# Performance work log

Measured on AMD Instinct MI355X. Metric: run time of the kernel, lower is better.

Reference implementation:

```python
import jax
import jax.numpy as jnp
import numpy as np
from jax.scipy.linalg import expm

H = 2048   # hidden_size
R = 1      # low-rank dimension
B = 2048   # batch of independent (h, x) pairs


def _glorot(key, shape):
    return jax.random.uniform(key, shape, minval=-1.0, maxval=1.0) * jnp.sqrt(2.0 / sum(shape))


def setup_inputs() -> dict:
    key = jax.random.key(0)
    k1, k2, k3, k4, k5, k6 = jax.random.split(key, 6)
    return {
        "h": jax.random.normal(k5, (B, H), dtype=jnp.float32),
        "x": jax.random.normal(k6, (B, H), dtype=jnp.float32),
        # a_diag ~ U(-1, 0) * init_scale (10.0): negative real diagonal
        "a_diag": jax.random.uniform(k1, (H,), minval=-1.0, maxval=0.0) * 10.0,
        "p_vec": _glorot(k2, (H, R)),
        "q_vec": _glorot(k3, (H, R)),
        "b_mat": _glorot(k4, (H, H)),
        "delta": jnp.array(0.1, dtype=jnp.float32),
    }


def reference(h, x, a_diag, p_vec, q_vec, b_mat, delta):
    # A = diag(a_diag) + P Q^T  (DPLR structure, materialized dense as in source)
    A = jnp.diag(a_diag) + p_vec @ q_vec.T                       # [H, H]
    # Discretized state matrix: exp(delta * A)
    expA = expm(delta * A)                                       # [H, H]
    # Discretized input matrix: A^{-1} (exp(delta A) - I) B  (pinv as in source)
    A_inv = jnp.linalg.pinv(A)                                   # [H, H]
    B_disc = A_inv @ (expA - jnp.eye(H, dtype=A.dtype)) @ b_mat  # [H, H]
    # Batched recurrence step: A h + B x  for each row of h, x
    return h @ expA.T + x @ B_disc.T                             # [B, H]
```

## Files before the change

### kernel.cpp

```cpp
#include <hip/hip_runtime.h>

#define MAXM 16
#define NL_CAP 256
#define THETA 0.1f
#define SMEM_BYTES 36864

typedef unsigned short u16;
typedef u16 u16x8 __attribute__((ext_vector_type(8)));
typedef u16 u16x4 __attribute__((ext_vector_type(4)));
typedef __bf16 bf16x8 __attribute__((ext_vector_type(8)));
typedef float f32x4 __attribute__((ext_vector_type(4)));


__device__ __forceinline__ u16 f2bf(float f) {
    unsigned u = __float_as_uint(f);
    return (u16)((u + 0x7fffu + ((u >> 16) & 1u)) >> 16);
}

__global__ __launch_bounds__(256)
void conv_k(const float* __restrict__ x, const float* __restrict__ b,
            u16* __restrict__ xb, u16* __restrict__ bb, long nx, long nb)
{
    long i = ((long)blockIdx.x * 256 + threadIdx.x) * 4;
    if (i < nx) {
        float4 v = *(const float4*)&x[i];
        u16x4 o = {f2bf(v.x), f2bf(v.y), f2bf(v.z), f2bf(v.w)};
        *(u16x4*)&xb[i] = o;
    }
    if (i < nb) {
        float4 v = *(const float4*)&b[i];
        u16x4 o = {f2bf(v.x), f2bf(v.y), f2bf(v.z), f2bf(v.w)};
        *(u16x4*)&bb[i] = o;
    }
}


__device__ __forceinline__ double frcp(double den) {
    double r = (double)__builtin_amdgcn_rcpf((float)den);
    return fma(r, fma(-den, r, 1.0), r);
}


__device__ __forceinline__ void gload_lds16(const void* g, void* l) {
    __builtin_amdgcn_global_load_lds(
        (const __attribute__((address_space(1))) unsigned int*)g,
        (__attribute__((address_space(3))) unsigned int*)l, 16, 0, 0);
}

__device__ __forceinline__ void gemm_tile(u16* Al, u16* Bl, int tid, int bx, int by,
                                          const u16* __restrict__ A,
                                          const u16* __restrict__ B,
                                          float* __restrict__ C,
                                          int Ndim, int Kdim)
{
    const int bm = by * 128, bn = bx * 128;
    const int wv = tid >> 6, ln = tid & 63;
    const int wr = (wv >> 1) * 64, wc = (wv & 1) * 64;
    const int fr = ln & 15, fk = (ln >> 4) * 8;

    const int r0 = tid >> 2, c0 = (tid & 3) * 8;
    const u16* Ap0 = A + (size_t)(bm + r0) * Kdim + c0;
    const u16* Ap1 = Ap0 + (size_t)64 * Kdim;
    const u16* Bp0 = B + (size_t)(bn + r0) * Kdim + c0;
    const u16* Bp1 = Bp0 + (size_t)64 * Kdim;
    u16* AlW0 = Al + wv * 512;
    u16* AlW1 = Al + 2048 + wv * 512;
    u16* BlW0 = Bl + wv * 512;
    u16* BlW1 = Bl + 2048 + wv * 512;

    f32x4 acc[4][4];
#pragma unroll
    for (int m = 0; m < 4; ++m)
#pragma unroll
        for (int n = 0; n < 4; ++n) acc[m][n] = (f32x4)0.f;

    for (int kk = 0; kk < Kdim; kk += 32) {
        __syncthreads();
        gload_lds16(Ap0 + kk, AlW0);
        gload_lds16(Ap1 + kk, AlW1);
        gload_lds16(Bp0 + kk, BlW0);
        gload_lds16(Bp1 + kk, BlW1);
        __syncthreads();
        u16x8 af[4], bf[4];
#pragma unroll
        for (int m = 0; m < 4; ++m)
            af[m] = *(const u16x8*)&Al[(wr + m * 16 + fr) * 32 + fk];
#pragma unroll
        for (int n = 0; n < 4; ++n)
            bf[n] = *(const u16x8*)&Bl[(wc + n * 16 + fr) * 32 + fk];
#pragma unroll
        for (int m = 0; m < 4; ++m)
#pragma unroll
            for (int n = 0; n < 4; ++n)
                acc[m][n] = __builtin_amdgcn_mfma_f32_16x16x32_bf16(
                    __builtin_bit_cast(bf16x8, af[m]),
                    __builtin_bit_cast(bf16x8, bf[n]), acc[m][n], 0, 0, 0);
    }

    const int crow = (ln >> 4) * 4;
#pragma unroll
    for (int m = 0; m < 4; ++m)
#pragma unroll
        for (int n = 0; n < 4; ++n) {
            const size_t base = (size_t)(bm + wr + m * 16 + crow) * Ndim
                              + bn + wc + n * 16 + fr;
#pragma unroll
            for (int j = 0; j < 4; ++j)
                C[base + (size_t)j * Ndim] = acc[m][n][j];
        }
}

__global__ __launch_bounds__(256)
void bgemm_k(const u16* __restrict__ A, const u16* __restrict__ B,
             float* __restrict__ C, int Ndim, int Kdim)
{
    __shared__ __align__(16) unsigned char smem[SMEM_BYTES];
    gemm_tile((u16*)smem, (u16*)smem + 4096, threadIdx.x,
              blockIdx.x, blockIdx.y, A, B, C, Ndim, Kdim);
}


__global__ __launch_bounds__(256)
void g_sgemm_k(const float* __restrict__ A, const float* __restrict__ B,
               float* __restrict__ C, int Mdim, int Ndim, int Kdim)
{
    __shared__ __align__(16) float As[16][132];
    __shared__ __align__(16) float Bs[16][68];
    const int tid = threadIdx.x;
    const int tx = tid & 15, ty = tid >> 4;
    const int bn = blockIdx.x * 64, bm = blockIdx.y * 128;
    const int lrA = tid >> 1, lcA = (tid & 1) << 3;
    const int lrB = tid >> 2, lcB = (tid & 3) << 2;
    const float* Aptr = A + (size_t)(bm + lrA) * Kdim + lcA;
    const float* Bptr = B + (size_t)(bn + lrB) * Kdim + lcB;
    float4 a0 = *(const float4*)(Aptr);
    float4 a1 = *(const float4*)(Aptr + 4);
    float4 b0 = *(const float4*)(Bptr);
    float acc[8][4];
#pragma unroll
    for (int i = 0; i < 8; ++i)
#pragma unroll
        for (int j = 0; j < 4; ++j) acc[i][j] = 0.f;
    for (int kk = 0; kk < Kdim; kk += 16) {
        __syncthreads();
        As[lcA + 0][lrA] = a0.x; As[lcA + 1][lrA] = a0.y;
        As[lcA + 2][lrA] = a0.z; As[lcA + 3][lrA] = a0.w;
        As[lcA + 4][lrA] = a1.x; As[lcA + 5][lrA] = a1.y;
        As[lcA + 6][lrA] = a1.z; As[lcA + 7][lrA] = a1.w;
        Bs[lcB + 0][lrB] = b0.x; Bs[lcB + 1][lrB] = b0.y;
        Bs[lcB + 2][lrB] = b0.z; Bs[lcB + 3][lrB] = b0.w;
        __syncthreads();
        if (kk + 16 < Kdim) {
            a0 = *(const float4*)(Aptr + kk + 16);
            a1 = *(const float4*)(Aptr + kk + 20);
            b0 = *(const float4*)(Bptr + kk + 16);
        }
#pragma unroll
        for (int k = 0; k < 16; ++k) {
            const float4 av0 = *(const float4*)&As[k][ty * 8];
            const float4 av1 = *(const float4*)&As[k][ty * 8 + 4];
            const float4 bv  = *(const float4*)&Bs[k][tx * 4];
            const float avf[8] = {av0.x, av0.y, av0.z, av0.w, av1.x, av1.y, av1.z, av1.w};
            const float bvf[4] = {bv.x, bv.y, bv.z, bv.w};
#pragma unroll
            for (int i = 0; i < 8; ++i)
#pragma unroll
                for (int j = 0; j < 4; ++j) acc[i][j] += avf[i] * bvf[j];
        }
    }
#pragma unroll
    for (int i = 0; i < 8; ++i) {
        const int r = bm + ty * 8 + i;
        float4 v = {acc[i][0], acc[i][1], acc[i][2], acc[i][3]};
        *(float4*)&C[(size_t)r * Ndim + bn + tx * 4] = v;
    }
}


__device__ __forceinline__ double wsum(double x) {
#pragma unroll
    for (int m = 32; m; m >>= 1) x += __shfl_xor(x, m, 64);
    return x;
}
__device__ __forceinline__ float wsumf(float x) {
#pragma unroll
    for (int m = 32; m; m >>= 1) x += __shfl_xor(x, m, 64);
    return x;
}

__device__ __forceinline__ int inert(double s11, double s12, double s22,
                                     double dc, double cS)
{
    double b00 = cS - s11, b01 = -1.0 - s12, b11 = -s22;
    double det = b00 * b11 - b01 * b01, tr = b00 + b11;
    int neg = (det > 0.0) ? ((tr < 0.0) ? 2 : 0) : 1;
    return (int)(dc + 0.5) + neg - 1;
}

__device__ __forceinline__ int lane_evalN32(float tf, double td, int n4,
    const float4* l0, const float4* l1, const float4* l2,
    const double* pc, bool poly, double cS,
    double& g11o, double& g12o, double& g22o)
{
    float s11 = 0.f, s12 = 0.f, s22 = 0.f, dc = 0.f;
#pragma unroll 2
    for (int i = 0; i < n4; ++i) {
        const float4 d4 = l0[i], x4 = l1[i], y4 = l2[i];
        const float dd[4] = {d4.x, d4.y, d4.z, d4.w};
        const float xx[4] = {x4.x, x4.y, x4.z, x4.w};
        const float yy[4] = {y4.x, y4.y, y4.z, y4.w};
#pragma unroll
        for (int e = 0; e < 4; ++e) {
            float den = dd[e] - tf;
            float mag = fmaxf(fabsf(den), 1e-30f);
            den = (den < 0.f) ? -mag : mag;
            const float inv = __builtin_amdgcn_rcpf(den);
            s11 = fmaf(xx[e] * xx[e], inv, s11);
            s12 = fmaf(xx[e] * yy[e], inv, s12);
            s22 = fmaf(yy[e] * yy[e], inv, s22);
            if (dd[e] < tf) dc += 1.f;
        }
    }
    double S11 = (double)s11, S12 = (double)s12, S22 = (double)s22;
    if (poly) {
        S11 += pc[0] + td * (pc[3] + td * (pc[6] + td * pc[9]));
        S12 += pc[1] + td * (pc[4] + td * (pc[7] + td * pc[10]));
        S22 += pc[2] + td * (pc[5] + td * (pc[8] + td * pc[11]));
    }
    g11o = S11; g12o = S12; g22o = S22;
    return inert(S11, S12, S22, (double)dc, cS);
}

__device__ void spec256(unsigned char* smem, int tid,
                        const float* __restrict__ av, const float* __restrict__ pv,
                        const float* __restrict__ qv, double* __restrict__ hdr,
                        float* __restrict__ V)
{
    float* sd2 = (float*)smem;
    float* sw1 = sd2 + 2048;
    float* sw2 = sw1 + 2048;
    float* nl0 = sw2 + 2048;
    float* nl1 = nl0 + NL_CAP;
    float* nl2 = nl1 + NL_CAP;
    double* dsh = (double*)(nl2 + NL_CAP);
    int* ish = (int*)(dsh + 192);

    const int lane = tid & 63, wv = tid >> 6;
    const int j0 = tid * 8;

    float d2r[8], w1r[8], w2r[8];
    double cS = 0, n1 = 0, n2 = 0, mx = 0;
#pragma unroll
    for (int h = 0; h < 2; ++h) {
        float4 aa = *(const float4*)&av[j0 + h * 4];
        float4 pp = *(const float4*)&pv[j0 + h * 4];
        float4 qq = *(const float4*)&qv[j0 + h * 4];
        const float a4[4] = {aa.x, aa.y, aa.z, aa.w};
        const float p4[4] = {pp.x, pp.y, pp.z, pp.w};
        const float q4[4] = {qq.x, qq.y, qq.z, qq.w};
#pragma unroll
        for (int e = 0; e < 4; ++e) {
            const int ix = h * 4 + e;
            d2r[ix] = a4[e] * a4[e];
            w1r[ix] = a4[e] * p4[e];
            w2r[ix] = q4[e];
            sd2[j0 + ix] = d2r[ix]; sw1[j0 + ix] = w1r[ix]; sw2[j0 + ix] = w2r[ix];
            cS += (double)p4[e] * p4[e];
            n1 += (double)w1r[ix] * w1r[ix];
            n2 += (double)w2r[ix] * w2r[ix];
            mx = fmax(mx, (double)d2r[ix]);
        }
    }
    cS = wsum(cS); n1 = wsum(n1); n2 = wsum(n2);
#pragma unroll
    for (int m_ = 32; m_; m_ >>= 1) mx = fmax(mx, __shfl_xor(mx, m_, 64));
    __syncthreads();
    if (lane == 0) { dsh[wv] = cS; dsh[4 + wv] = n1; dsh[8 + wv] = n2; dsh[12 + wv] = mx; }
    __syncthreads();
    cS = 0; n1 = 0; n2 = 0; mx = 0;
    for (int w = 0; w < 4; ++w) {
        cS += dsh[w]; n1 += dsh[4 + w]; n2 += dsh[8 + w];
        mx = fmax(mx, dsh[12 + w]);
    }
    __syncthreads();

    double lo = 0.0;
    double hi = mx + 0.5 * (cS + sqrt(cS * cS + 4.0)) * (n1 + n2) + 1.0;
    for (int r = 0; r < 8; ++r) {
        const double td = lo + (hi - lo) * (double)(wv + 1) / 5.0;
        const float tf = (float)td;
        float s11 = 0.f, s12 = 0.f, s22 = 0.f, dc = 0.f;
        for (int i4 = lane; i4 < 512; i4 += 64) {
            const float4 dd = ((const float4*)sd2)[i4];
            const float4 e1 = ((const float4*)sw1)[i4];
            const float4 e2 = ((const float4*)sw2)[i4];
            const float df[4] = {dd.x, dd.y, dd.z, dd.w};
            const float f1[4] = {e1.x, e1.y, e1.z, e1.w};
            const float f2[4] = {e2.x, e2.y, e2.z, e2.w};
#pragma unroll
            for (int e = 0; e < 4; ++e) {
                float den = df[e] - tf;
                float mag = fmaxf(fabsf(den), 1e-30f);
                den = (den < 0.f) ? -mag : mag;
                const float inv = __builtin_amdgcn_rcpf(den);
                s11 = fmaf(f1[e] * f1[e], inv, s11);
                s12 = fmaf(f1[e] * f2[e], inv, s12);
                s22 = fmaf(f2[e] * f2[e], inv, s22);
                if (df[e] < tf) dc += 1.f;
            }
        }
        s11 = wsumf(s11); s12 = wsumf(s12); s22 = wsumf(s22); dc = wsumf(dc);
        if (lane == 0)
            ish[wv] = inert((double)s11, (double)s12, (double)s22, (double)dc, cS);
        __syncthreads();
        double nlo = lo, nhi = hi;
        for (int i = 0; i < 4; ++i) {
            double ti = lo + (hi - lo) * (double)(i + 1) / 5.0;
            if (ish[i] >= 2048) { if (ti < nhi) nhi = ti; }
            else                { if (ti > nlo) nlo = ti; }
        }
        lo = nlo; hi = nhi;
        __syncthreads();
    }
    const double lmax = 0.5 * (lo + hi);
    const double rc = 10.0 * 2048.0 * 1.1920928955078125e-07;
    const double cut2 = rc * rc * lmax;

    int flags = 0, lc = 0;
#pragma unroll
    for (int e = 0; e < 8; ++e)
        if (d2r[e] < THETA) { flags |= (1 << e); ++lc; }
    int sc = lc;
#pragma unroll
    for (int off = 1; off < 64; off <<= 1) {
        int y = __shfl_up(sc, off, 64);
        if (lane >= off) sc += y;
    }
    const int wtot = __shfl(sc, 63, 64);
    const int excl = sc - lc;
    if (lane == 0) ish[4 + wv] = wtot;
    __syncthreads();
    int base = excl;
    for (int w = 0; w < wv; ++w) base += ish[4 + w];
    int cnt = 0;
    for (int w = 0; w < 4; ++w) cnt += ish[4 + w];
    {
        int pos = base;
#pragma unroll
        for (int e = 0; e < 8; ++e) {
            if (flags & (1 << e)) {
                if (pos < NL_CAP) { nl0[pos] = d2r[e]; nl1[pos] = w1r[e]; nl2[pos] = w2r[e]; }
                ++pos;
            }
        }
    }
    const int cntPad = (cnt + 7) & ~7;
    if (tid == 0) {
        for (int i = cnt; i < cntPad && i < NL_CAP; ++i) {
            nl0[i] = 1e30f; nl1[i] = 0.f; nl2[i] = 0.f;
        }
        ish[8] = cnt; ish[10] = cntPad >> 2;
    }

    double cf[12];
#pragma unroll
    for (int c = 0; c < 12; ++c) cf[c] = 0;
#pragma unroll
    for (int e = 0; e < 8; ++e) {
        if (d2r[e] >= THETA) {
            double id = frcp((double)d2r[e]);
            double b1 = (double)w1r[e], b2 = (double)w2r[e];
            double x11 = b1 * b1, x12 = b1 * b2, x22 = b2 * b2;
            double f = id;
            cf[0] += x11 * f; cf[1]  += x12 * f; cf[2]  += x22 * f; f *= id;
            cf[3] += x11 * f; cf[4]  += x12 * f; cf[5]  += x22 * f; f *= id;
            cf[6] += x11 * f; cf[7]  += x12 * f; cf[8]  += x22 * f; f *= id;
            cf[9] += x11 * f; cf[10] += x12 * f; cf[11] += x22 * f;
        }
    }
#pragma unroll
    for (int c = 0; c < 12; ++c) cf[c] = wsum(cf[c]);
    if (lane == 0) {
        double* dw = &dsh[16 + wv * 12];
#pragma unroll
        for (int c = 0; c < 12; ++c) dw[c] = cf[c];
    }
    __syncthreads();
    if (tid < 12) {
        double s = 0;
        for (int w = 0; w < 4; ++w) s += dsh[16 + w * 12 + tid];
        dsh[96 + tid] = s;
    }
    __syncthreads();

    cnt = ish[8];
    const bool nearOK = (cnt <= NL_CAP - 8);
    const float4* l0 = nearOK ? (const float4*)nl0 : (const float4*)sd2;
    const float4* l1 = nearOK ? (const float4*)nl1 : (const float4*)sw1;
    const float4* l2 = nearOK ? (const float4*)nl2 : (const float4*)sw2;
    const int n4 = nearOK ? ish[10] : 512;
    const bool poly = nearOK;
    const double* pcoef = &dsh[96];

    double zg1, zg2, zg3;
    if (wv == 0) {
        int N = lane_evalN32((float)cut2, cut2, n4, l0, l1, l2, pcoef, poly, cS,
                             zg1, zg2, zg3);
        if (lane == 0) ish[9] = N;
    }
    __syncthreads();
    int m = ish[9];
    if (m < 0) m = 0;
    if (m > MAXM) m = MAXM;

    for (int k = wv; k < m; k += 4) {
        double klo = 0.0, khi = cut2;
        for (int r = 0; r < 3; ++r) {
            const double w = khi - klo;
            const double td = klo + w * (double)(lane + 1) / 65.0;
            int N = lane_evalN32((float)td, td, n4, l0, l1, l2, pcoef, poly, cS,
                                 zg1, zg2, zg3);
            unsigned long long mask = __ballot(N >= k + 1);
            int j = (mask == 0ull) ? 64 : (__ffsll(mask) - 1);
            double nk = (j == 64) ? khi : (klo + w * (double)(j + 1) / 65.0);
            klo = klo + w * (double)j / 65.0;
            khi = nk;
        }
        const double lam = 0.5 * (klo + khi);
        double g11, g12, g22;
        lane_evalN32((float)lam, lam, n4, l0, l1, l2, pcoef, poly, cS, g11, g12, g22);
        const double m00 = 1.0 + g12, m01 = g11 + cS * g12;
        const double m10 = g22,       m11 = 1.0 + g12 + cS * g22;
        double y1, y2;
        if (m00 * m00 + m01 * m01 >= m10 * m10 + m11 * m11) { y1 = m01; y2 = -m00; }
        else                                                { y1 = m11; y2 = -m10; }
        if (lane == 0) {
            dsh[112 + 3 * k]     = lam;
            dsh[112 + 3 * k + 1] = y2;
            dsh[112 + 3 * k + 2] = y1 + cS * y2;
        }
    }
    __syncthreads();

    for (int k = 0; k < m; ++k) {
        const double lam = dsh[112 + 3 * k];
        const double z1 = dsh[112 + 3 * k + 1], z2 = dsh[112 + 3 * k + 2];
        double vr[8], pn = 0;
#pragma unroll
        for (int e = 0; e < 8; ++e) {
            double den = (double)d2r[e] - lam;
            if (fabs(den) < 1e-25) den = (den < 0 ? -1e-25 : 1e-25);
            vr[e] = ((double)w1r[e] * z1 + (double)w2r[e] * z2) * frcp(den);
            pn += vr[e] * vr[e];
        }
        pn = wsum(pn);
        if (lane == 0) dsh[160 + wv] = pn;
        __syncthreads();
        double tot = 0;
        for (int w = 0; w < 4; ++w) tot += dsh[160 + w];
        const double inv = 1.0 / sqrt(tot);
        float o0[8];
#pragma unroll
        for (int e = 0; e < 8; ++e) o0[e] = (float)(vr[e] * inv);
        *(float4*)&V[(size_t)k * 2048 + j0]     = *(float4*)&o0[0];
        *(float4*)&V[(size_t)k * 2048 + j0 + 4] = *(float4*)&o0[4];
        __syncthreads();
    }

    if (tid == 0) { hdr[0] = lmax; hdr[1] = cut2; hdr[2] = (double)m; hdr[3] = cS; }
}


__global__ __launch_bounds__(256)
void fat_k(const u16* __restrict__ A, const u16* __restrict__ B,
           float* __restrict__ C, int Ndim, int Kdim, int ntiles, int nbx,
           const float* __restrict__ av, const float* __restrict__ pv,
           const float* __restrict__ qv, double* __restrict__ hdr,
           float* __restrict__ V)
{
    __shared__ __align__(16) unsigned char smem[SMEM_BYTES];
    const int bid = blockIdx.x;
    if (bid == 0) {
        spec256(smem, threadIdx.x, av, pv, qv, hdr, V);
        return;
    }
    if (bid - 1 >= ntiles) return;
    const int t = bid - 1;
    gemm_tile((u16*)smem, (u16*)smem + 4096, threadIdx.x,
              t % nbx, t / nbx, A, B, C, Ndim, Kdim);
}


__global__ __launch_bounds__(256, 2)
void series_k(float* __restrict__ io, const float* __restrict__ hm,
              const float* __restrict__ qv, const float* __restrict__ pv,
              const float* __restrict__ av, const float* __restrict__ delta,
              const float* __restrict__ V, const double* __restrict__ hdr,
              int useTrunc)
{
    const int lane = threadIdx.x & 63;
    const int row = blockIdx.x * 4 + (threadIdx.x >> 6);
    const float d = delta[0];
    const int m = useTrunc ? (int)hdr[2] : 0;

    float q[32], p[32], a[32], t[32], o[32];
    float* iorow = io + (size_t)row * 2048;
#pragma unroll
    for (int cc = 0; cc < 8; ++cc) {
        const int j = cc * 256 + lane * 4;
        *(float4*)&q[cc * 4] = *(const float4*)&qv[j];
        *(float4*)&p[cc * 4] = *(const float4*)&pv[j];
        *(float4*)&a[cc * 4] = *(const float4*)&av[j];
        *(float4*)&t[cc * 4] = *(const float4*)&iorow[j];
    }
#pragma unroll
    for (int e = 0; e < 32; ++e) o[e] = t[e];

    float cf = 1.f;
    for (int k = 1; k <= 13; ++k) {
        float s = 0.f;
#pragma unroll
        for (int e = 0; e < 32; ++e) s += t[e] * q[e];
#pragma unroll
        for (int msk = 32; msk; msk >>= 1) s += __shfl_xor(s, msk, 64);
        cf /= (float)(k + 1);
        const float ds = d * s;
#pragma unroll
        for (int e = 0; e < 32; ++e) { t[e] = d * a[e] * t[e] + ds * p[e]; o[e] += cf * t[e]; }
    }
#pragma unroll
    for (int e = 0; e < 32; ++e) o[e] *= d;

    for (int k = 0; k < m; ++k) {
        const float* vr = V + (size_t)k * 2048;
        float vk[32];
#pragma unroll
        for (int cc = 0; cc < 8; ++cc)
            *(float4*)&vk[cc * 4] = *(const float4*)&vr[cc * 256 + lane * 4];
        float s = 0.f;
#pragma unroll
        for (int e = 0; e < 32; ++e) s += o[e] * vk[e];
#pragma unroll
        for (int msk = 32; msk; msk >>= 1) s += __shfl_xor(s, msk, 64);
#pragma unroll
        for (int e = 0; e < 32; ++e) o[e] -= s * vk[e];
    }

    const float* hrow = hm + (size_t)row * 2048;
#pragma unroll
    for (int cc = 0; cc < 8; ++cc)
        *(float4*)&t[cc * 4] = *(const float4*)&hrow[cc * 256 + lane * 4];
#pragma unroll
    for (int e = 0; e < 32; ++e) o[e] += t[e];
    cf = 1.f;
    for (int k = 1; k <= 14; ++k) {
        float s = 0.f;
#pragma unroll
        for (int e = 0; e < 32; ++e) s += t[e] * q[e];
#pragma unroll
        for (int msk = 32; msk; msk >>= 1) s += __shfl_xor(s, msk, 64);
        cf /= (float)k;
        const float ds = d * s;
#pragma unroll
        for (int e = 0; e < 32; ++e) { t[e] = d * a[e] * t[e] + ds * p[e]; o[e] += cf * t[e]; }
    }
#pragma unroll
    for (int cc = 0; cc < 8; ++cc)
        *(float4*)&iorow[cc * 256 + lane * 4] = *(const float4*)&o[cc * 4];
}


extern "C" void kernel_launch(void* const* d_in, const int* in_sizes, int n_in,
                              void* d_out, int out_size, void* d_ws, size_t ws_size,
                              hipStream_t stream)
{
    const float* hmat  = (const float*)d_in[0];
    const float* xmat  = (const float*)d_in[1];
    const float* adiag = (const float*)d_in[2];
    const float* pvec  = (const float*)d_in[3];
    const float* qvec  = (const float*)d_in[4];
    const float* bmat  = (const float*)d_in[5];
    const float* delta = (const float*)d_in[6];
    float* out = (float*)d_out;

    const int H  = in_sizes[2];
    const int Bb = in_sizes[0] / H;
    const size_t SZ = (size_t)Bb * H;
    const size_t HH = (size_t)H * H;

    double* hdr = (double*)d_ws;
    float* V = (float*)(hdr + 8);
    u16* xb = (u16*)(V + (size_t)MAXM * H);
    u16* bb = xb + SZ;

    const size_t needSpec = 64 + (size_t)MAXM * H * sizeof(float);
    const size_t needFull = needSpec + (SZ + HH) * sizeof(u16);
    const bool doTrunc = (H == 2048) && (ws_size >= needSpec);
    const bool doBf16  = (ws_size >= needFull) && (H % 128 == 0) && (Bb % 128 == 0);

    dim3 blk256(256);
    const int nbx = H / 128;
    const int ntiles = nbx * (Bb / 128);

    if (doBf16) {
        const long nmax = (long)(SZ > HH ? SZ : HH);
        const int cg = (int)((nmax / 4 + 255) / 256);
        conv_k<<<cg, blk256, 0, stream>>>(xmat, bmat, xb, bb, (long)SZ, (long)HH);
        if (doTrunc) {
            fat_k<<<1 + ntiles, blk256, 0, stream>>>(xb, bb, out, H, H, ntiles, nbx,
                                                     adiag, pvec, qvec, hdr, V);
        } else {
            dim3 gg(nbx, Bb / 128);
            bgemm_k<<<gg, blk256, 0, stream>>>(xb, bb, out, H, H);
        }
    } else {
        if (doTrunc)
            fat_k<<<1, blk256, 0, stream>>>(nullptr, nullptr, out, H, H, 0, 1,
                                            adiag, pvec, qvec, hdr, V);
        dim3 gg(H / 64, Bb / 128);
        g_sgemm_k<<<gg, blk256, 0, stream>>>(xmat, bmat, out, Bb, H, H);
    }

    series_k<<<Bb / 4, blk256, 0, stream>>>(out, hmat, qvec, pvec, adiag, delta,
                                            V, hdr, doTrunc ? 1 : 0);
}
```

Before: 91.42 us.

## Split-K the bf16 x·Bᵀ GEMM into two halves summed in series kernel

```diff
diff --git a/kernel.cpp b/kernel.cpp
--- a/kernel.cpp
+++ b/kernel.cpp
@@ -51,7 +51,7 @@
                                           const u16* __restrict__ A,
                                           const u16* __restrict__ B,
                                           float* __restrict__ C,
-                                          int Ndim, int Kdim)
+                                          int Ndim, int Kstride, int Klen)
 {
     const int bm = by * 128, bn = bx * 128;
     const int wv = tid >> 6, ln = tid & 63;
@@ -59,10 +59,10 @@
     const int fr = ln & 15, fk = (ln >> 4) * 8;
 
     const int r0 = tid >> 2, c0 = (tid & 3) * 8;
-    const u16* Ap0 = A + (size_t)(bm + r0) * Kdim + c0;
-    const u16* Ap1 = Ap0 + (size_t)64 * Kdim;
-    const u16* Bp0 = B + (size_t)(bn + r0) * Kdim + c0;
-    const u16* Bp1 = Bp0 + (size_t)64 * Kdim;
+    const u16* Ap0 = A + (size_t)(bm + r0) * Kstride + c0;
+    const u16* Ap1 = Ap0 + (size_t)64 * Kstride;
+    const u16* Bp0 = B + (size_t)(bn + r0) * Kstride + c0;
+    const u16* Bp1 = Bp0 + (size_t)64 * Kstride;
     u16* AlW0 = Al + wv * 512;
     u16* AlW1 = Al + 2048 + wv * 512;
     u16* BlW0 = Bl + wv * 512;
@@ -74,7 +74,7 @@
 #pragma unroll
         for (int n = 0; n < 4; ++n) acc[m][n] = (f32x4)0.f;
 
-    for (int kk = 0; kk < Kdim; kk += 32) {
+    for (int kk = 0; kk < Klen; kk += 32) {
         __syncthreads();
         gload_lds16(Ap0 + kk, AlW0);
         gload_lds16(Ap1 + kk, AlW1);
@@ -116,7 +116,7 @@
 {
     __shared__ __align__(16) unsigned char smem[SMEM_BYTES];
     gemm_tile((u16*)smem, (u16*)smem + 4096, threadIdx.x,
-              blockIdx.x, blockIdx.y, A, B, C, Ndim, Kdim);
+              blockIdx.x, blockIdx.y, A, B, C, Ndim, Kdim, Kdim);
 }
 
 
@@ -473,7 +473,8 @@
 
 __global__ __launch_bounds__(256)
 void fat_k(const u16* __restrict__ A, const u16* __restrict__ B,
-           float* __restrict__ C, int Ndim, int Kdim, int ntiles, int nbx,
+           float* __restrict__ C0, float* __restrict__ C1,
+           int Ndim, int Kdim, int ntiles, int nbx, int nsplit,
            const float* __restrict__ av, const float* __restrict__ pv,
            const float* __restrict__ qv, double* __restrict__ hdr,
            float* __restrict__ V)
@@ -484,15 +485,21 @@
         spec256(smem, threadIdx.x, av, pv, qv, hdr, V);
         return;
     }
-    if (bid - 1 >= ntiles) return;
     const int t = bid - 1;
+    if (t >= ntiles * nsplit) return;
+    const int ks = t / ntiles;
+    const int tt = t - ks * ntiles;
+    const int Klen = Kdim / nsplit;
     gemm_tile((u16*)smem, (u16*)smem + 4096, threadIdx.x,
-              t % nbx, t / nbx, A, B, C, Ndim, Kdim);
+              tt % nbx, tt / nbx,
+              A + (size_t)ks * Klen, B + (size_t)ks * Klen,
+              ks ? C1 : C0, Ndim, Kdim, Klen);
 }
 
 
 __global__ __launch_bounds__(256, 2)
-void series_k(float* __restrict__ io, const float* __restrict__ hm,
+void series_k(float* __restrict__ io, const float* __restrict__ io2, int addP,
+              const float* __restrict__ hm,
               const float* __restrict__ qv, const float* __restrict__ pv,
               const float* __restrict__ av, const float* __restrict__ delta,
               const float* __restrict__ V, const double* __restrict__ hdr,
@@ -505,13 +512,19 @@
 
     float q[32], p[32], a[32], t[32], o[32];
     float* iorow = io + (size_t)row * 2048;
+    const float* io2row = io2 + (size_t)row * 2048;
 #pragma unroll
     for (int cc = 0; cc < 8; ++cc) {
         const int j = cc * 256 + lane * 4;
         *(float4*)&q[cc * 4] = *(const float4*)&qv[j];
         *(float4*)&p[cc * 4] = *(const float4*)&pv[j];
         *(float4*)&a[cc * 4] = *(const float4*)&av[j];
-        *(float4*)&t[cc * 4] = *(const float4*)&iorow[j];
+        float4 u0 = *(const float4*)&iorow[j];
+        if (addP) {
+            const float4 u1 = *(const float4*)&io2row[j];
+            u0.x += u1.x; u0.y += u1.y; u0.z += u1.z; u0.w += u1.w;
+        }
+        *(float4*)&t[cc * 4] = u0;
     }
 #pragma unroll
     for (int e = 0; e < 32; ++e) o[e] = t[e];
@@ -592,11 +605,14 @@
     float* V = (float*)(hdr + 8);
     u16* xb = (u16*)(V + (size_t)MAXM * H);
     u16* bb = xb + SZ;
-
-    const size_t needSpec = 64 + (size_t)MAXM * H * sizeof(float);
-    const size_t needFull = needSpec + (SZ + HH) * sizeof(u16);
+    float* C1 = (float*)(bb + HH);
+
+    const size_t needSpec  = 64 + (size_t)MAXM * H * sizeof(float);
+    const size_t needFull  = needSpec + (SZ + HH) * sizeof(u16);
+    const size_t needSplit = needFull + SZ * sizeof(float);
     const bool doTrunc = (H == 2048) && (ws_size >= needSpec);
     const bool doBf16  = (ws_size >= needFull) && (H % 128 == 0) && (Bb % 128 == 0);
+    const bool doSplit = doBf16 && doTrunc && (ws_size >= needSplit) && (H % 64 == 0);
 
     dim3 blk256(256);
     const int nbx = H / 128;
@@ -607,20 +623,25 @@
         const int cg = (int)((nmax / 4 + 255) / 256);
         conv_k<<<cg, blk256, 0, stream>>>(xmat, bmat, xb, bb, (long)SZ, (long)HH);
         if (doTrunc) {
-            fat_k<<<1 + ntiles, blk256, 0, stream>>>(xb, bb, out, H, H, ntiles, nbx,
-                                                     adiag, pvec, qvec, hdr, V);
+            const int nsplit = doSplit ? 2 : 1;
+            fat_k<<<1 + ntiles * nsplit, blk256, 0, stream>>>(
+                xb, bb, out, C1, H, H, ntiles, nbx, nsplit,
+                adiag, pvec, qvec, hdr, V);
         } else {
             dim3 gg(nbx, Bb / 128);
             bgemm_k<<<gg, blk256, 0, stream>>>(xb, bb, out, H, H);
         }
     } else {
         if (doTrunc)
-            fat_k<<<1, blk256, 0, stream>>>(nullptr, nullptr, out, H, H, 0, 1,
+            fat_k<<<1, blk256, 0, stream>>>(nullptr, nullptr, out, nullptr,
+                                            H, H, 0, 1, 1,
                                             adiag, pvec, qvec, hdr, V);
         dim3 gg(H / 64, Bb / 128);
         g_sgemm_k<<<gg, blk256, 0, stream>>>(xmat, bmat, out, Bb, H, H);
     }
 
-    series_k<<<Bb / 4, blk256, 0, stream>>>(out, hmat, qvec, pvec, adiag, delta,
+    series_k<<<Bb / 4, blk256, 0, stream>>>(out, doSplit ? C1 : out,
+                                            doSplit ? 1 : 0,
+                                            hmat, qvec, pvec, adiag, delta,
                                             V, hdr, doTrunc ? 1 : 0);
 }
```

Result: no change. 91.22 us (-0.2%).
